# Performance work log

Measured on AMD Instinct MI355X. Metric: run time of the kernel, lower is better.

The kernel has to match this reference:

```python
import jax, jax.numpy as jnp
import numpy as np

ND, NS = 50000, 30000
FD = FS = 256
H = 256
E = 1000000
EL = 200000


def _lin_init(key, fan_in, fan_out):
    # torch Linear default: U(-1/sqrt(fan_in), 1/sqrt(fan_in)) for W and b
    kw, kb = jax.random.split(key)
    bound = 1.0 / np.sqrt(fan_in)
    W = jax.random.uniform(kw, (fan_in, fan_out), jnp.float32, -bound, bound)
    b = jax.random.uniform(kb, (fan_out,), jnp.float32, -bound, bound)
    return W, b


def setup_inputs() -> dict:
    key = jax.random.key(0)
    ks = jax.random.split(key, 16)
    x_drug = jax.random.normal(ks[0], (ND, FD), jnp.float32)
    x_disease = jax.random.normal(ks[1], (NS, FS), jnp.float32)
    edge_src = jax.random.randint(ks[2], (E,), 0, ND, jnp.int64)
    edge_dst = jax.random.randint(ks[3], (E,), 0, NS, jnp.int64)
    label_row = jax.random.randint(ks[4], (EL,), 0, ND, jnp.int64)
    label_col = jax.random.randint(ks[5], (EL,), 0, NS, jnp.int64)
    # SAGEConv params per layer per edge type: lin_l (on aggregated src, with bias),
    # lin_r (on dst root, no bias). Edge types: ds = drug->disease, sd = disease->drug (rev).
    Wl1_ds, bl1_ds = _lin_init(ks[6], FD, H)
    Wr1_ds, _ = _lin_init(ks[7], FS, H)
    Wl1_sd, bl1_sd = _lin_init(ks[8], FS, H)
    Wr1_sd, _ = _lin_init(ks[9], FD, H)
    Wl2_ds, bl2_ds = _lin_init(ks[10], H, H)
    Wr2_ds, _ = _lin_init(ks[11], H, H)
    Wl2_sd, bl2_sd = _lin_init(ks[12], H, H)
    Wr2_sd, _ = _lin_init(ks[13], H, H)
    Wdec1, bdec1 = _lin_init(ks[14], 2 * H, H)
    Wdec2, bdec2 = _lin_init(ks[15], H, 1)
    return dict(x_drug=x_drug, x_disease=x_disease,
                edge_src=edge_src, edge_dst=edge_dst,
                label_row=label_row, label_col=label_col,
                Wl1_ds=Wl1_ds, bl1_ds=bl1_ds, Wr1_ds=Wr1_ds,
                Wl1_sd=Wl1_sd, bl1_sd=bl1_sd, Wr1_sd=Wr1_sd,
                Wl2_ds=Wl2_ds, bl2_ds=bl2_ds, Wr2_ds=Wr2_ds,
                Wl2_sd=Wl2_sd, bl2_sd=bl2_sd, Wr2_sd=Wr2_sd,
                Wdec1=Wdec1, bdec1=bdec1, Wdec2=Wdec2, bdec2=bdec2)


def _mean_agg(x_src, src, dst, n_dst):
    # gather source features per edge, mean-scatter into destinations
    msg = x_src[src]                                         # [E, F]
    s = jax.ops.segment_sum(msg, dst, num_segments=n_dst)    # [n_dst, F]
    cnt = jax.ops.segment_sum(jnp.ones_like(dst, x_src.dtype), dst, num_segments=n_dst)
    return s / jnp.maximum(cnt, 1.0)[:, None]


def _sage_layer(x_drug, x_dis, src, dst,
                Wl_ds, bl_ds, Wr_ds, Wl_sd, bl_sd, Wr_sd):
    z_dis = _mean_agg(x_drug, src, dst, NS) @ Wl_ds + bl_ds + x_dis @ Wr_ds
    z_drug = _mean_agg(x_dis, dst, src, ND) @ Wl_sd + bl_sd + x_drug @ Wr_sd
    return z_drug, z_dis


def reference(x_drug, x_disease, edge_src, edge_dst, label_row, label_col,
              Wl1_ds, bl1_ds, Wr1_ds, Wl1_sd, bl1_sd, Wr1_sd,
              Wl2_ds, bl2_ds, Wr2_ds, Wl2_sd, bl2_sd, Wr2_sd,
              Wdec1, bdec1, Wdec2, bdec2):
    # layer 1 (relu)
    zd, zs = _sage_layer(x_drug, x_disease, edge_src, edge_dst,
                         Wl1_ds, bl1_ds, Wr1_ds, Wl1_sd, bl1_sd, Wr1_sd)
    zd, zs = jax.nn.relu(zd), jax.nn.relu(zs)
    # layer 2 (no relu, last layer)
    zd, zs = _sage_layer(zd, zs, edge_src, edge_dst,
                         Wl2_ds, bl2_ds, Wr2_ds, Wl2_sd, bl2_sd, Wr2_sd)
    # edge decoder
    z = jnp.concatenate([zd[label_row], zs[label_col]], axis=-1)  # [EL, 2H]
    h = jax.nn.relu(z @ Wdec1 + bdec1)
    out = (h @ Wdec2 + bdec2).reshape(-1)
    return out
```

## Files before the change

### kernel.cpp

```cpp
#include <hip/hip_runtime.h>
#include <hip/hip_bf16.h>

#define ND 50000
#define NS 30000
#define NE 1000000
#define EL 200000
#define NTOT (NS + ND)
#define SCAN_BLK ((NTOT + 1023) / 1024)

typedef short short8 __attribute__((ext_vector_type(8)));
typedef float f32x4 __attribute__((ext_vector_type(4)));

__device__ __forceinline__ float b2f(unsigned short u) {
    union { unsigned int i; float f; } c; c.i = ((unsigned int)u) << 16; return c.f;
}
__device__ __forceinline__ unsigned short f2b(float f) {
    __hip_bfloat16 h = __float2bfloat16(f);
    union { __hip_bfloat16 h; unsigned short u; } c; c.h = h; return c.u;
}

__device__ __forceinline__ void gload_lds16(const unsigned short* g, unsigned short* l) {
    __builtin_amdgcn_global_load_lds(
        (const __attribute__((address_space(1))) unsigned int*)g,
        (__attribute__((address_space(3))) unsigned int*)l, 16, 0, 0);
}


__global__ void zero_kernel(int* a, int n) {
    int i = blockIdx.x * blockDim.x + threadIdx.x;
    if (i < n) a[i] = 0;
}

__global__ void rank_kernel(const int* __restrict__ src, const int* __restrict__ dst,
                            int* cnt_drug, int* cnt_dis,
                            unsigned short* __restrict__ rank_sd,
                            unsigned short* __restrict__ rank_ds, int n) {
    int i = blockIdx.x * blockDim.x + threadIdx.x;
    if (i < n) {
        int s = src[i], d = dst[i];
        rank_ds[i] = (unsigned short)atomicAdd(&cnt_dis[d], 1);
        rank_sd[i] = (unsigned short)atomicAdd(&cnt_drug[s], 1);
    }
}

__global__ __launch_bounds__(256) void scan_part(const int* __restrict__ cnt,
                                                 int* __restrict__ bsum) {
    __shared__ int red[4];
    int t = threadIdx.x, lane = t & 63, wid = t >> 6;
    int base = blockIdx.x * 1024 + t * 4;
    int s = 0;
    if (base < NTOT) {
        int4 c = *reinterpret_cast<const int4*>(cnt + base);
        s = c.x + c.y + c.z + c.w;
    }
#pragma unroll
    for (int off = 32; off; off >>= 1) s += __shfl_down(s, off);
    if (lane == 0) red[wid] = s;
    __syncthreads();
    if (t == 0) bsum[blockIdx.x] = red[0] + red[1] + red[2] + red[3];
}

__global__ void scan_top(int* bsum, int nb) {
    int lane = threadIdx.x;
    int a0 = lane < nb ? bsum[lane] : 0;
    int a1 = (64 + lane) < nb ? bsum[64 + lane] : 0;
    int i0 = a0, i1 = a1;
#pragma unroll
    for (int off = 1; off < 64; off <<= 1) {
        int t0 = __shfl_up(i0, off);
        int t1 = __shfl_up(i1, off);
        if (lane >= off) { i0 += t0; i1 += t1; }
    }
    int tot0 = __shfl(i0, 63);
    if (lane < nb) bsum[lane] = i0 - a0;
    if (64 + lane < nb) bsum[64 + lane] = tot0 + i1 - a1;
}

__global__ __launch_bounds__(256) void scan_emit(const int* __restrict__ cnt,
                                                 const int* __restrict__ boff,
                                                 int* __restrict__ row_dis,
                                                 int* __restrict__ row_drug,
                                                 float* __restrict__ inv_dis,
                                                 float* __restrict__ inv_drug) {
    __shared__ int wsum[4];
    int t = threadIdx.x, lane = t & 63, wid = t >> 6;
    int base = blockIdx.x * 1024 + t * 4;
    int4 c = make_int4(0, 0, 0, 0);
    if (base < NTOT) c = *reinterpret_cast<const int4*>(cnt + base);
    int sl = c.x + c.y + c.z + c.w;
    int sc = sl;
#pragma unroll
    for (int off = 1; off < 64; off <<= 1) {
        int tv = __shfl_up(sc, off);
        if (lane >= off) sc += tv;
    }
    if (lane == 63) wsum[wid] = sc;
    __syncthreads();
    int woff = 0;
    for (int w2 = 0; w2 < wid; ++w2) woff += wsum[w2];
    int run = boff[blockIdx.x] + woff + (sc - sl);
    int cc[4] = { c.x, c.y, c.z, c.w };
    if (base < NTOT) {
#pragma unroll
        for (int k = 0; k < 4; ++k) {
            int i = base + k;
            float iv = 1.0f / (float)(cc[k] > 1 ? cc[k] : 1);
            if (i < NS) { row_dis[i] = run; inv_dis[i] = iv; }
            else        { row_drug[i - NS] = run - NE; inv_drug[i - NS] = iv; }
            run += cc[k];
        }
    }
    if (blockIdx.x == 0 && t == 0) { row_dis[NS] = NE; row_drug[ND] = NE; }
}

__global__ void place_kernel(const int* __restrict__ src, const int* __restrict__ dst,
                             const int* __restrict__ row_drug, const int* __restrict__ row_dis,
                             const unsigned short* __restrict__ rank_sd,
                             const unsigned short* __restrict__ rank_ds,
                             unsigned short* __restrict__ val_sd,
                             unsigned short* __restrict__ val_ds, int n) {
    int i = blockIdx.x * blockDim.x + threadIdx.x;
    if (i < n) {
        int s = src[i], d = dst[i];
        val_ds[row_dis[d] + (int)rank_ds[i]] = (unsigned short)s;
        val_sd[row_drug[s] + (int)rank_sd[i]] = (unsigned short)d;
    }
}


__global__ void convert_x(const float* __restrict__ xd, const float* __restrict__ xs,
                          unsigned short* __restrict__ outd, unsigned short* __restrict__ outs) {
    int i = (blockIdx.x * 256 + threadIdx.x) * 4;
    const int NDE = ND * 256;
    if (i < NDE) {
        float4 v = *reinterpret_cast<const float4*>(xd + i);
        ushort4 o; o.x = f2b(v.x); o.y = f2b(v.y); o.z = f2b(v.z); o.w = f2b(v.w);
        *reinterpret_cast<ushort4*>(outd + i) = o;
    } else {
        int j = i - NDE;
        float4 v = *reinterpret_cast<const float4*>(xs + j);
        ushort4 o; o.x = f2b(v.x); o.y = f2b(v.y); o.z = f2b(v.z); o.w = f2b(v.w);
        *reinterpret_cast<ushort4*>(outs + j) = o;
    }
}

struct W10 { const float* p[10]; };

__global__ void transpose_w(W10 s, unsigned short* __restrict__ dst) {
    int o = blockIdx.x * 256 + threadIdx.x;
    int mat = o >> 16, idx = o & 65535;
    int n = idx >> 8, k = idx & 255;
    dst[o] = f2b(s.p[mat][k * 256 + n]);
}


__global__ __launch_bounds__(256) void agg_bf2(const unsigned short* __restrict__ srcDis,
                                               const unsigned short* __restrict__ srcDrug,
                                               const int* __restrict__ row_dis,
                                               const int* __restrict__ row_drug,
                                               const unsigned short* __restrict__ val_ds,
                                               const unsigned short* __restrict__ val_sd,
                                               const float* __restrict__ inv_dis,
                                               const float* __restrict__ inv_drug,
                                               unsigned short* __restrict__ outDis,
                                               unsigned short* __restrict__ outDrug) {
    int wid = threadIdx.x >> 6, lane = threadIdx.x & 63;
    int node = blockIdx.x * 4 + wid;
    const int half = lane >> 5;
    const int sub = lane & 31;
    const unsigned short* xsrc; const int* row; const unsigned short* vals;
    const float* inv; unsigned short* outp;
    if (node < NS) {
        xsrc = srcDis; row = row_dis; vals = val_ds; inv = inv_dis; outp = outDis;
    } else {
        node -= NS;
        if (node >= ND) return;
        xsrc = srcDrug; row = row_drug; vals = val_sd; inv = inv_drug; outp = outDrug;
    }
    const int beg = row[node], end = row[node + 1];
    const int off = sub * 8;
    float a[8] = {};
    int j = beg;
    for (; j + 8 <= end; j += 8) {
        int r0 = vals[j     + half];
        int r1 = vals[j + 2 + half];
        int r2 = vals[j + 4 + half];
        int r3 = vals[j + 6 + half];
        short8 v0 = *reinterpret_cast<const short8*>(xsrc + r0 * 256 + off);
        short8 v1 = *reinterpret_cast<const short8*>(xsrc + r1 * 256 + off);
        short8 v2 = *reinterpret_cast<const short8*>(xsrc + r2 * 256 + off);
        short8 v3 = *reinterpret_cast<const short8*>(xsrc + r3 * 256 + off);
#pragma unroll
        for (int k = 0; k < 8; ++k)
            a[k] += b2f((unsigned short)v0[k]) + b2f((unsigned short)v1[k])
                  + b2f((unsigned short)v2[k]) + b2f((unsigned short)v3[k]);
    }
    for (; j + 2 <= end; j += 2) {
        int r = vals[j + half];
        short8 v = *reinterpret_cast<const short8*>(xsrc + r * 256 + off);
#pragma unroll
        for (int k = 0; k < 8; ++k) a[k] += b2f((unsigned short)v[k]);
    }
    if (j < end && half == 0) {
        int r = vals[j];
        short8 v = *reinterpret_cast<const short8*>(xsrc + r * 256 + off);
#pragma unroll
        for (int k = 0; k < 8; ++k) a[k] += b2f((unsigned short)v[k]);
    }
#pragma unroll
    for (int k = 0; k < 8; ++k) a[k] += __shfl_xor(a[k], 32);
    if (half == 0) {
        const float iv = inv[node];
        short8 o;
#pragma unroll
        for (int k = 0; k < 8; ++k) o[k] = (short)f2b(a[k] * iv);
        *reinterpret_cast<short8*>(outp + node * 256 + off) = o;
    }
}


struct GemmSeg {
    const unsigned short* A1;
    const unsigned short* A2;
    const unsigned short* B1t;
    const unsigned short* B2t;
    const float* bias;
    unsigned short* C;
    int M; int relu; int nblk; int nsteps;
};

__global__ __launch_bounds__(256) void gemm_lds(GemmSeg sa, GemmSeg sb) {
    __shared__ unsigned short As[128 * 64];
    __shared__ unsigned short Bs[128 * 64];
    GemmSeg s;
    int bx = blockIdx.x;
    if (bx < sa.nblk) s = sa;
    else { s = sb; bx -= sa.nblk; }

    const int t = threadIdx.x;
    const int lane = t & 63, w = t >> 6;
    const int wr = w >> 1, wc = w & 1;
    const int fr = lane & 15, g = lane >> 4;
    const int bm0 = bx * 128;
    const int n0b = (int)blockIdx.y * 128;
    const int M = s.M;
    const int r8 = lane >> 3, slotL = lane & 7;

    f32x4 acc[4][4];
#pragma unroll
    for (int m = 0; m < 4; ++m)
#pragma unroll
        for (int n = 0; n < 4; ++n)
            acc[m][n] = (f32x4){0.f, 0.f, 0.f, 0.f};

    for (int st = 0; st < s.nsteps; ++st) {
        const int k0 = (st & 3) * 64;
        const unsigned short* Ap = (st & 4) ? s.A2 : s.A1;
        const unsigned short* Bp = (st & 4) ? s.B2t : s.B1t;
#pragma unroll
        for (int j = 0; j < 4; ++j) {
            const int is = w * 4 + j;
            const int row = is * 8 + r8;
            const int sl = slotL ^ (row & 7);
            int ra = bm0 + row; if (ra >= M) ra = M - 1;
            gload_lds16(Ap + (size_t)ra * 256 + k0 + sl * 8, &As[is * 512]);
            gload_lds16(Bp + (size_t)(n0b + row) * 256 + k0 + sl * 8, &Bs[is * 512]);
        }
        __syncthreads();
#pragma unroll
        for (int kc = 0; kc < 2; ++kc) {
            const int q = kc * 4 + g;
            short8 a[4], b[4];
#pragma unroll
            for (int n = 0; n < 4; ++n) {
                const int br = wc * 64 + n * 16 + fr;
                b[n] = *reinterpret_cast<const short8*>(&Bs[br * 64 + (q ^ (fr & 7)) * 8]);
            }
#pragma unroll
            for (int m = 0; m < 4; ++m) {
                const int ar = wr * 64 + m * 16 + fr;
                a[m] = *reinterpret_cast<const short8*>(&As[ar * 64 + (q ^ (fr & 7)) * 8]);
            }
#pragma unroll
            for (int m = 0; m < 4; ++m)
#pragma unroll
                for (int n = 0; n < 4; ++n)
                    acc[m][n] = __builtin_amdgcn_mfma_f32_16x16x32_bf16(a[m], b[n], acc[m][n], 0, 0, 0);
        }
        __syncthreads();
    }

#pragma unroll
    for (int n = 0; n < 4; ++n) {
        const int col = n0b + wc * 64 + n * 16 + fr;
        const float bv = s.bias ? s.bias[col] : 0.0f;
#pragma unroll
        for (int m = 0; m < 4; ++m) {
#pragma unroll
            for (int r = 0; r < 4; ++r) {
                int row = bm0 + wr * 64 + m * 16 + g * 4 + r;
                if (row < M) {
                    float v = acc[m][n][r] + bv;
                    if (s.relu) v = fmaxf(v, 0.f);
                    s.C[row * 256 + col] = f2b(v);
                }
            }
        }
    }
}


__global__ __launch_bounds__(256) void dec_edge(const unsigned short* __restrict__ Pd,
                                                const unsigned short* __restrict__ Ps,
                                                const int* __restrict__ lrow,
                                                const int* __restrict__ lcol,
                                                const float* __restrict__ b1,
                                                const float* __restrict__ w2,
                                                const float* __restrict__ b2,
                                                float* __restrict__ outp, int n) {
    int wid = threadIdx.x >> 6, lane = threadIdx.x & 63;
    int e = blockIdx.x * 4 + wid;
    if (e >= n) return;
    int r = lrow[e], c = lcol[e];
    const int off = lane * 4;
    ushort4 pd = *reinterpret_cast<const ushort4*>(Pd + r * 256 + off);
    ushort4 ps = *reinterpret_cast<const ushort4*>(Ps + c * 256 + off);
    float4 bb = *reinterpret_cast<const float4*>(b1 + off);
    float4 ww = *reinterpret_cast<const float4*>(w2 + off);
    float s = 0.f;
    s += fmaxf(b2f(pd.x) + b2f(ps.x) + bb.x, 0.f) * ww.x;
    s += fmaxf(b2f(pd.y) + b2f(ps.y) + bb.y, 0.f) * ww.y;
    s += fmaxf(b2f(pd.z) + b2f(ps.z) + bb.z, 0.f) * ww.z;
    s += fmaxf(b2f(pd.w) + b2f(ps.w) + bb.w, 0.f) * ww.w;
#pragma unroll
    for (int o = 32; o; o >>= 1) s += __shfl_down(s, o);
    if (lane == 0) outp[e] = s + b2[0];
}


extern "C" void kernel_launch(void* const* d_in, const int* in_sizes, int n_in,
                              void* d_out, int out_size, void* d_ws, size_t ws_size,
                              hipStream_t stream) {
    const float* x_drug = (const float*)d_in[0];
    const float* x_dis  = (const float*)d_in[1];
    const int* esrc = (const int*)d_in[2];
    const int* edst = (const int*)d_in[3];
    const int* lrow = (const int*)d_in[4];
    const int* lcol = (const int*)d_in[5];
    const float* Wl1_ds = (const float*)d_in[6];
    const float* bl1_ds = (const float*)d_in[7];
    const float* Wr1_ds = (const float*)d_in[8];
    const float* Wl1_sd = (const float*)d_in[9];
    const float* bl1_sd = (const float*)d_in[10];
    const float* Wr1_sd = (const float*)d_in[11];
    const float* Wl2_ds = (const float*)d_in[12];
    const float* bl2_ds = (const float*)d_in[13];
    const float* Wr2_ds = (const float*)d_in[14];
    const float* Wl2_sd = (const float*)d_in[15];
    const float* bl2_sd = (const float*)d_in[16];
    const float* Wr2_sd = (const float*)d_in[17];
    const float* Wdec1 = (const float*)d_in[18];
    const float* bdec1 = (const float*)d_in[19];
    const float* Wdec2 = (const float*)d_in[20];
    const float* bdec2 = (const float*)d_in[21];
    float* outp = (float*)d_out;

    char* ws = (char*)d_ws;
    size_t off = 0;
    auto alloc = [&](size_t bytes) -> void* {
        void* p = ws + off;
        off = (off + bytes + 255) & ~(size_t)255;
        return p;
    };
    int* cnt       = (int*)alloc((size_t)NTOT * 4);
    int* bsum      = (int*)alloc((size_t)SCAN_BLK * 4);
    int* row_dis   = (int*)alloc((size_t)(NS + 1) * 4);
    int* row_drug  = (int*)alloc((size_t)(ND + 1) * 4);
    float* inv_dis = (float*)alloc((size_t)NS * 4);
    float* inv_drug= (float*)alloc((size_t)ND * 4);
    unsigned short* rank_ds = (unsigned short*)alloc((size_t)NE * 2);
    unsigned short* rank_sd = (unsigned short*)alloc((size_t)NE * 2);
    unsigned short* val_ds  = (unsigned short*)alloc((size_t)NE * 2);
    unsigned short* val_sd  = (unsigned short*)alloc((size_t)NE * 2);
    unsigned short* Wt   = (unsigned short*)alloc((size_t)10 * 65536 * 2);
    unsigned short* xd_b = (unsigned short*)alloc((size_t)ND * 256 * 2);
    unsigned short* xs_b = (unsigned short*)alloc((size_t)NS * 256 * 2);
    unsigned short* aggs = (unsigned short*)alloc((size_t)NS * 256 * 2);
    unsigned short* aggd = (unsigned short*)alloc((size_t)ND * 256 * 2);
    unsigned short* zd1  = (unsigned short*)alloc((size_t)ND * 256 * 2);
    unsigned short* zs1  = (unsigned short*)alloc((size_t)NS * 256 * 2);
    unsigned short* zd2  = (unsigned short*)alloc((size_t)ND * 256 * 2);
    unsigned short* zs2  = (unsigned short*)alloc((size_t)NS * 256 * 2);
    unsigned short* Pd   = (unsigned short*)alloc((size_t)ND * 256 * 2);
    unsigned short* Ps   = (unsigned short*)alloc((size_t)NS * 256 * 2);
    int* cnt_dis = cnt;
    int* cnt_drug = cnt + NS;

    convert_x<<<(ND + NS) * 256 / 1024, 256, 0, stream>>>(x_drug, x_dis, xd_b, xs_b);
    W10 wsrc;
    wsrc.p[0] = Wl1_ds; wsrc.p[1] = Wr1_ds; wsrc.p[2] = Wl1_sd; wsrc.p[3] = Wr1_sd;
    wsrc.p[4] = Wl2_ds; wsrc.p[5] = Wr2_ds; wsrc.p[6] = Wl2_sd; wsrc.p[7] = Wr2_sd;
    wsrc.p[8] = Wdec1;
    wsrc.p[9] = Wdec1 + 256 * 256;
    transpose_w<<<2560, 256, 0, stream>>>(wsrc, Wt);
    unsigned short* WT[10];
    for (int i = 0; i < 10; ++i) WT[i] = Wt + (size_t)i * 65536;

    zero_kernel<<<(NTOT + 255) / 256, 256, 0, stream>>>(cnt, NTOT);
    rank_kernel<<<(NE + 255) / 256, 256, 0, stream>>>(esrc, edst, cnt_drug, cnt_dis,
                                                      rank_sd, rank_ds, NE);
    scan_part<<<SCAN_BLK, 256, 0, stream>>>(cnt, bsum);
    scan_top<<<1, 64, 0, stream>>>(bsum, SCAN_BLK);
    scan_emit<<<SCAN_BLK, 256, 0, stream>>>(cnt, bsum, row_dis, row_drug, inv_dis, inv_drug);
    place_kernel<<<(NE + 255) / 256, 256, 0, stream>>>(esrc, edst, row_drug, row_dis,
                                                       rank_sd, rank_ds, val_sd, val_ds, NE);

    const int AGG_GRID = (NTOT + 3) / 4;
    const int NB_NS = (NS + 127) / 128, NB_ND = (ND + 127) / 128;
    dim3 gemm_grid(NB_NS + NB_ND, 2);

    agg_bf2<<<AGG_GRID, 256, 0, stream>>>(xd_b, xs_b, row_dis, row_drug, val_ds, val_sd,
                                          inv_dis, inv_drug, aggs, aggd);
    {
        GemmSeg a = { aggs, xs_b, WT[0], WT[1], bl1_ds, zs1, NS, 1, NB_NS, 8 };
        GemmSeg b = { aggd, xd_b, WT[2], WT[3], bl1_sd, zd1, ND, 1, NB_ND, 8 };
        gemm_lds<<<gemm_grid, 256, 0, stream>>>(a, b);
    }

    agg_bf2<<<AGG_GRID, 256, 0, stream>>>(zd1, zs1, row_dis, row_drug, val_ds, val_sd,
                                          inv_dis, inv_drug, aggs, aggd);
    {
        GemmSeg a = { aggs, zs1, WT[4], WT[5], bl2_ds, zs2, NS, 0, NB_NS, 8 };
        GemmSeg b = { aggd, zd1, WT[6], WT[7], bl2_sd, zd2, ND, 0, NB_ND, 8 };
        gemm_lds<<<gemm_grid, 256, 0, stream>>>(a, b);
    }

    {
        GemmSeg a = { zd2, nullptr, WT[8], nullptr, nullptr, Pd, ND, 0, NB_ND, 4 };
        GemmSeg b = { zs2, nullptr, WT[9], nullptr, nullptr, Ps, NS, 0, NB_NS, 4 };
        gemm_lds<<<gemm_grid, 256, 0, stream>>>(a, b);
    }
    dec_edge<<<(EL + 3) / 4, 256, 0, stream>>>(Pd, Ps, lrow, lcol, bdec1, Wdec2, bdec2, outp, EL);
}
```

Baseline: 575.7 us.

## Split aggregation by feature chunk per XCD with persistent atomic work queues

Replaces the per-node wave aggregation with a persistent kernel that reads the XCC ID and splits the 256-wide feature dimension into eight 32-column chunks. Each chunk is preferentially processed by blocks on one XCD, so that XCD's L2 only has to cache one slice of the source feature table. Blocks pull 32-node groups from per-chunk atomic counters, then move on to other chunks to balance load. The cost is narrower 8-byte gathers, repeated reads of the edge index lists for every chunk, and two __syncthreads plus one atomic per work item.

```diff
diff --git a/kernel.cpp b/kernel.cpp
--- a/kernel.cpp
+++ b/kernel.cpp
@@ -7,6 +7,8 @@
 #define EL 200000
 #define NTOT (NS + ND)
 #define SCAN_BLK ((NTOT + 1023) / 1024)
+#define NCHUNK 8
+#define NGRP (NTOT / 32)
 
 typedef short short8 __attribute__((ext_vector_type(8)));
 typedef float f32x4 __attribute__((ext_vector_type(4)));
@@ -153,8 +155,7 @@
     dst[o] = f2b(s.p[mat][k * 256 + n]);
 }
 
-
-__global__ __launch_bounds__(256) void agg_bf2(const unsigned short* __restrict__ srcDis,
+__global__ __launch_bounds__(256) void agg_xcd(const unsigned short* __restrict__ srcDis,
                                                const unsigned short* __restrict__ srcDrug,
                                                const int* __restrict__ row_dis,
                                                const int* __restrict__ row_drug,
@@ -163,58 +164,57 @@
                                                const float* __restrict__ inv_dis,
                                                const float* __restrict__ inv_drug,
                                                unsigned short* __restrict__ outDis,
-                                               unsigned short* __restrict__ outDrug) {
-    int wid = threadIdx.x >> 6, lane = threadIdx.x & 63;
-    int node = blockIdx.x * 4 + wid;
-    const int half = lane >> 5;
-    const int sub = lane & 31;
-    const unsigned short* xsrc; const int* row; const unsigned short* vals;
-    const float* inv; unsigned short* outp;
-    if (node < NS) {
-        xsrc = srcDis; row = row_dis; vals = val_ds; inv = inv_dis; outp = outDis;
-    } else {
-        node -= NS;
-        if (node >= ND) return;
-        xsrc = srcDrug; row = row_drug; vals = val_sd; inv = inv_drug; outp = outDrug;
-    }
-    const int beg = row[node], end = row[node + 1];
-    const int off = sub * 8;
-    float a[8] = {};
-    int j = beg;
-    for (; j + 8 <= end; j += 8) {
-        int r0 = vals[j     + half];
-        int r1 = vals[j + 2 + half];
-        int r2 = vals[j + 4 + half];
-        int r3 = vals[j + 6 + half];
-        short8 v0 = *reinterpret_cast<const short8*>(xsrc + r0 * 256 + off);
-        short8 v1 = *reinterpret_cast<const short8*>(xsrc + r1 * 256 + off);
-        short8 v2 = *reinterpret_cast<const short8*>(xsrc + r2 * 256 + off);
-        short8 v3 = *reinterpret_cast<const short8*>(xsrc + r3 * 256 + off);
-#pragma unroll
-        for (int k = 0; k < 8; ++k)
-            a[k] += b2f((unsigned short)v0[k]) + b2f((unsigned short)v1[k])
-                  + b2f((unsigned short)v2[k]) + b2f((unsigned short)v3[k]);
-    }
-    for (; j + 2 <= end; j += 2) {
-        int r = vals[j + half];
-        short8 v = *reinterpret_cast<const short8*>(xsrc + r * 256 + off);
-#pragma unroll
-        for (int k = 0; k < 8; ++k) a[k] += b2f((unsigned short)v[k]);
-    }
-    if (j < end && half == 0) {
-        int r = vals[j];
-        short8 v = *reinterpret_cast<const short8*>(xsrc + r * 256 + off);
-#pragma unroll
-        for (int k = 0; k < 8; ++k) a[k] += b2f((unsigned short)v[k]);
-    }
-#pragma unroll
-    for (int k = 0; k < 8; ++k) a[k] += __shfl_xor(a[k], 32);
-    if (half == 0) {
-        const float iv = inv[node];
-        short8 o;
-#pragma unroll
-        for (int k = 0; k < 8; ++k) o[k] = (short)f2b(a[k] * iv);
-        *reinterpret_cast<short8*>(outp + node * 256 + off) = o;
+                                               unsigned short* __restrict__ outDrug,
+                                               int* __restrict__ qcnt) {
+    unsigned xcc;
+    asm volatile("s_getreg_b32 %0, hwreg(HW_REG_XCC_ID)" : "=s"(xcc));
+    xcc &= 7;
+    const int slot = threadIdx.x >> 3;
+    const int sub = threadIdx.x & 7;
+    __shared__ int s_item;
+
+    for (int qi = 0; qi < NCHUNK; ++qi) {
+        const int q = (xcc + qi) & 7;
+        for (;;) {
+            if (threadIdx.x == 0) s_item = atomicAdd(&qcnt[q], 1);
+            __syncthreads();
+            const int g = s_item;
+            __syncthreads();
+            if (g >= NGRP) break;
+            int node = g * 32 + slot;
+            const unsigned short* xsrc; const int* row; const unsigned short* vals;
+            const float* inv; unsigned short* outp;
+            if (node < NS) {
+                xsrc = srcDis; row = row_dis; vals = val_ds; inv = inv_dis; outp = outDis;
+            } else {
+                node -= NS;
+                xsrc = srcDrug; row = row_drug; vals = val_sd; inv = inv_drug; outp = outDrug;
+            }
+            const int beg = row[node], end = row[node + 1];
+            const int off = q * 32 + sub * 4;
+            float a0 = 0.f, a1 = 0.f, a2 = 0.f, a3 = 0.f;
+            int j = beg;
+            for (; j + 4 <= end; j += 4) {
+                int s0 = vals[j], s1 = vals[j + 1], s2 = vals[j + 2], s3 = vals[j + 3];
+                ushort4 v0 = *reinterpret_cast<const ushort4*>(xsrc + s0 * 256 + off);
+                ushort4 v1 = *reinterpret_cast<const ushort4*>(xsrc + s1 * 256 + off);
+                ushort4 v2 = *reinterpret_cast<const ushort4*>(xsrc + s2 * 256 + off);
+                ushort4 v3 = *reinterpret_cast<const ushort4*>(xsrc + s3 * 256 + off);
+                a0 += b2f(v0.x) + b2f(v1.x) + b2f(v2.x) + b2f(v3.x);
+                a1 += b2f(v0.y) + b2f(v1.y) + b2f(v2.y) + b2f(v3.y);
+                a2 += b2f(v0.z) + b2f(v1.z) + b2f(v2.z) + b2f(v3.z);
+                a3 += b2f(v0.w) + b2f(v1.w) + b2f(v2.w) + b2f(v3.w);
+            }
+            for (; j < end; ++j) {
+                int s = vals[j];
+                ushort4 v = *reinterpret_cast<const ushort4*>(xsrc + s * 256 + off);
+                a0 += b2f(v.x); a1 += b2f(v.y); a2 += b2f(v.z); a3 += b2f(v.w);
+            }
+            const float iv = inv[node];
+            ushort4 o;
+            o.x = f2b(a0 * iv); o.y = f2b(a1 * iv); o.z = f2b(a2 * iv); o.w = f2b(a3 * iv);
+            *reinterpret_cast<ushort4*>(outp + node * 256 + off) = o;
+        }
     }
 }
 
@@ -372,7 +372,7 @@
         off = (off + bytes + 255) & ~(size_t)255;
         return p;
     };
-    int* cnt       = (int*)alloc((size_t)NTOT * 4);
+    int* cnt       = (int*)alloc((size_t)(NTOT + 16) * 4);
     int* bsum      = (int*)alloc((size_t)SCAN_BLK * 4);
     int* row_dis   = (int*)alloc((size_t)(NS + 1) * 4);
     int* row_drug  = (int*)alloc((size_t)(ND + 1) * 4);
@@ -395,6 +395,8 @@
     unsigned short* Ps   = (unsigned short*)alloc((size_t)NS * 256 * 2);
     int* cnt_dis = cnt;
     int* cnt_drug = cnt + NS;
+    int* qcnt1 = cnt + NTOT;
+    int* qcnt2 = cnt + NTOT + 8;
 
     convert_x<<<(ND + NS) * 256 / 1024, 256, 0, stream>>>(x_drug, x_dis, xd_b, xs_b);
     W10 wsrc;
@@ -406,7 +408,7 @@
     unsigned short* WT[10];
     for (int i = 0; i < 10; ++i) WT[i] = Wt + (size_t)i * 65536;
 
-    zero_kernel<<<(NTOT + 255) / 256, 256, 0, stream>>>(cnt, NTOT);
+    zero_kernel<<<(NTOT + 16 + 255) / 256, 256, 0, stream>>>(cnt, NTOT + 16);
     rank_kernel<<<(NE + 255) / 256, 256, 0, stream>>>(esrc, edst, cnt_drug, cnt_dis,
                                                       rank_sd, rank_ds, NE);
     scan_part<<<SCAN_BLK, 256, 0, stream>>>(cnt, bsum);
@@ -415,20 +417,20 @@
     place_kernel<<<(NE + 255) / 256, 256, 0, stream>>>(esrc, edst, row_drug, row_dis,
                                                        rank_sd, rank_ds, val_sd, val_ds, NE);
 
-    const int AGG_GRID = (NTOT + 3) / 4;
+    const int AGG_GRID = 2048;
     const int NB_NS = (NS + 127) / 128, NB_ND = (ND + 127) / 128;
     dim3 gemm_grid(NB_NS + NB_ND, 2);
 
-    agg_bf2<<<AGG_GRID, 256, 0, stream>>>(xd_b, xs_b, row_dis, row_drug, val_ds, val_sd,
-                                          inv_dis, inv_drug, aggs, aggd);
+    agg_xcd<<<AGG_GRID, 256, 0, stream>>>(xd_b, xs_b, row_dis, row_drug, val_ds, val_sd,
+                                          inv_dis, inv_drug, aggs, aggd, qcnt1);
     {
         GemmSeg a = { aggs, xs_b, WT[0], WT[1], bl1_ds, zs1, NS, 1, NB_NS, 8 };
         GemmSeg b = { aggd, xd_b, WT[2], WT[3], bl1_sd, zd1, ND, 1, NB_ND, 8 };
         gemm_lds<<<gemm_grid, 256, 0, stream>>>(a, b);
     }
 
-    agg_bf2<<<AGG_GRID, 256, 0, stream>>>(zd1, zs1, row_dis, row_drug, val_ds, val_sd,
-                                          inv_dis, inv_drug, aggs, aggd);
+    agg_xcd<<<AGG_GRID, 256, 0, stream>>>(zd1, zs1, row_dis, row_drug, val_ds, val_sd,
+                                          inv_dis, inv_drug, aggs, aggd, qcnt2);
     {
         GemmSeg a = { aggs, zs1, WT[4], WT[5], bl2_ds, zs2, NS, 0, NB_NS, 8 };
         GemmSeg b = { aggd, zd1, WT[6], WT[7], bl2_sd, zd2, ND, 0, NB_ND, 8 };
```

Result: slower. 1.228 ms (+113.3%).

## Double-buffer LDS tiles in gemm_lds to prefetch next k-step

Applied to the files above, without the earlier changes.

Splits the GEMM's shared-memory A/B tiles into two buffers and issues the global-to-LDS loads for the next k-step before computing on the current one. Row offsets are precomputed once outside the loop. This aims to hide global load latency behind MFMA work, at the cost of doubling LDS usage per block, which may lower occupancy.

```diff
diff --git a/kernel.cpp b/kernel.cpp
--- a/kernel.cpp
+++ b/kernel.cpp
@@ -230,8 +230,8 @@
 };
 
 __global__ __launch_bounds__(256) void gemm_lds(GemmSeg sa, GemmSeg sb) {
-    __shared__ unsigned short As[128 * 64];
-    __shared__ unsigned short Bs[128 * 64];
+    __shared__ unsigned short As[2][128 * 64];
+    __shared__ unsigned short Bs[2][128 * 64];
     GemmSeg s;
     int bx = blockIdx.x;
     if (bx < sa.nblk) s = sa;
@@ -246,6 +246,17 @@
     const int M = s.M;
     const int r8 = lane >> 3, slotL = lane & 7;
 
+    int raOff[4]; int rbOff[4];
+#pragma unroll
+    for (int j = 0; j < 4; ++j) {
+        const int is = w * 4 + j;
+        const int row = is * 8 + r8;
+        const int sl = slotL ^ (row & 7);
+        int ra = bm0 + row; if (ra >= M) ra = M - 1;
+        raOff[j] = ra * 256 + sl * 8;
+        rbOff[j] = (n0b + row) * 256 + sl * 8;
+    }
+
     f32x4 acc[4][4];
 #pragma unroll
     for (int m = 0; m < 4; ++m)
@@ -253,20 +264,32 @@
         for (int n = 0; n < 4; ++n)
             acc[m][n] = (f32x4){0.f, 0.f, 0.f, 0.f};
 
-    for (int st = 0; st < s.nsteps; ++st) {
-        const int k0 = (st & 3) * 64;
-        const unsigned short* Ap = (st & 4) ? s.A2 : s.A1;
-        const unsigned short* Bp = (st & 4) ? s.B2t : s.B1t;
+    const int nsteps = s.nsteps;
+    {
+        const unsigned short* Ap = s.A1;
+        const unsigned short* Bp = s.B1t;
 #pragma unroll
         for (int j = 0; j < 4; ++j) {
             const int is = w * 4 + j;
-            const int row = is * 8 + r8;
-            const int sl = slotL ^ (row & 7);
-            int ra = bm0 + row; if (ra >= M) ra = M - 1;
-            gload_lds16(Ap + (size_t)ra * 256 + k0 + sl * 8, &As[is * 512]);
-            gload_lds16(Bp + (size_t)(n0b + row) * 256 + k0 + sl * 8, &Bs[is * 512]);
+            gload_lds16(Ap + raOff[j], &As[0][is * 512]);
+            gload_lds16(Bp + rbOff[j], &Bs[0][is * 512]);
         }
-        __syncthreads();
+    }
+    __syncthreads();
+
+    for (int st = 0; st < nsteps; ++st) {
+        const int cur = st & 1;
+        if (st + 1 < nsteps) {
+            const int k1 = ((st + 1) & 3) * 64;
+            const unsigned short* Ap = ((st + 1) & 4) ? s.A2 : s.A1;
+            const unsigned short* Bp = ((st + 1) & 4) ? s.B2t : s.B1t;
+#pragma unroll
+            for (int j = 0; j < 4; ++j) {
+                const int is = w * 4 + j;
+                gload_lds16(Ap + raOff[j] + k1, &As[cur ^ 1][is * 512]);
+                gload_lds16(Bp + rbOff[j] + k1, &Bs[cur ^ 1][is * 512]);
+            }
+        }
 #pragma unroll
         for (int kc = 0; kc < 2; ++kc) {
             const int q = kc * 4 + g;
@@ -274,12 +297,12 @@
 #pragma unroll
             for (int n = 0; n < 4; ++n) {
                 const int br = wc * 64 + n * 16 + fr;
-                b[n] = *reinterpret_cast<const short8*>(&Bs[br * 64 + (q ^ (fr & 7)) * 8]);
+                b[n] = *reinterpret_cast<const short8*>(&Bs[cur][br * 64 + (q ^ (fr & 7)) * 8]);
             }
 #pragma unroll
             for (int m = 0; m < 4; ++m) {
                 const int ar = wr * 64 + m * 16 + fr;
-                a[m] = *reinterpret_cast<const short8*>(&As[ar * 64 + (q ^ (fr & 7)) * 8]);
+                a[m] = *reinterpret_cast<const short8*>(&As[cur][ar * 64 + (q ^ (fr & 7)) * 8]);
             }
 #pragma unroll
             for (int m = 0; m < 4; ++m)
```

After: 600.5 us. 4.3% more time.

## Fold decoder first layer into layer-2 weights and merge prep kernels

Applied to the files above, without the earlier changes.

Precomputes the products of the layer-2 SAGE weights with the decoder's first-layer weight halves, plus the layer-2 biases times those halves. Layer 2 can then write the decoder projections Pd/Ps directly, removing the zd2/zs2 intermediates and one full GEMM pass. The rank, bf16 conversion, layer-1 weight transpose and weight-product computations are merged into one multi-role launch to cut launch overhead. The edge decoder now handles two edges per wavefront with 8-wide loads. Precomposing the weights in fp32 and then rounding to bf16 changes the rounding behaviour slightly.

```diff
diff --git a/kernel.cpp b/kernel.cpp
--- a/kernel.cpp
+++ b/kernel.cpp
@@ -8,6 +8,13 @@
 #define NTOT (NS + ND)
 #define SCAN_BLK ((NTOT + 1023) / 1024)
 
+#define RANK_BLKS ((NE + 255) / 256)
+#define CONV_BLKS 20000
+#define TRW4_BLKS 1024
+#define COMP_BLKS 64
+#define BIAS_BLKS 2
+#define MEGA_BLKS (RANK_BLKS + CONV_BLKS + TRW4_BLKS + COMP_BLKS + BIAS_BLKS)
+
 typedef short short8 __attribute__((ext_vector_type(8)));
 typedef float f32x4 __attribute__((ext_vector_type(4)));
 
@@ -25,23 +32,90 @@
         (__attribute__((address_space(3))) unsigned int*)l, 16, 0, 0);
 }
 
+struct WAll {
+    const float* w1[4];
+    const float* w2[4];
+    const float* wdec1;
+    const float* bl2_ds;
+    const float* bl2_sd;
+};
 
 __global__ void zero_kernel(int* a, int n) {
     int i = blockIdx.x * blockDim.x + threadIdx.x;
     if (i < n) a[i] = 0;
 }
 
-__global__ void rank_kernel(const int* __restrict__ src, const int* __restrict__ dst,
-                            int* cnt_drug, int* cnt_dis,
-                            unsigned short* __restrict__ rank_sd,
-                            unsigned short* __restrict__ rank_ds, int n) {
-    int i = blockIdx.x * blockDim.x + threadIdx.x;
-    if (i < n) {
-        int s = src[i], d = dst[i];
-        rank_ds[i] = (unsigned short)atomicAdd(&cnt_dis[d], 1);
-        rank_sd[i] = (unsigned short)atomicAdd(&cnt_drug[s], 1);
-    }
-}
+__global__ __launch_bounds__(256) void mega_prep(const int* __restrict__ esrc,
+                                                 const int* __restrict__ edst,
+                                                 int* cnt_drug, int* cnt_dis,
+                                                 unsigned short* __restrict__ rank_sd,
+                                                 unsigned short* __restrict__ rank_ds,
+                                                 const float* __restrict__ xd,
+                                                 const float* __restrict__ xs,
+                                                 unsigned short* __restrict__ xd_b,
+                                                 unsigned short* __restrict__ xs_b,
+                                                 WAll wa,
+                                                 unsigned short* __restrict__ Wt,
+                                                 float* __restrict__ cbuf) {
+    __shared__ float w2t[16][256];
+    const int b = blockIdx.x, t = threadIdx.x;
+    if (b < RANK_BLKS) {
+        int i = b * 256 + t;
+        if (i < NE) {
+            int s = esrc[i], d = edst[i];
+            rank_ds[i] = (unsigned short)atomicAdd(&cnt_dis[d], 1);
+            rank_sd[i] = (unsigned short)atomicAdd(&cnt_drug[s], 1);
+        }
+    } else if (b < RANK_BLKS + CONV_BLKS) {
+        int i = ((b - RANK_BLKS) * 256 + t) * 4;
+        const int NDE = ND * 256;
+        if (i < NDE) {
+            float4 v = *reinterpret_cast<const float4*>(xd + i);
+            ushort4 o; o.x = f2b(v.x); o.y = f2b(v.y); o.z = f2b(v.z); o.w = f2b(v.w);
+            *reinterpret_cast<ushort4*>(xd_b + i) = o;
+        } else {
+            int j = i - NDE;
+            float4 v = *reinterpret_cast<const float4*>(xs + j);
+            ushort4 o; o.x = f2b(v.x); o.y = f2b(v.y); o.z = f2b(v.z); o.w = f2b(v.w);
+            *reinterpret_cast<ushort4*>(xs_b + j) = o;
+        }
+    } else if (b < RANK_BLKS + CONV_BLKS + TRW4_BLKS) {
+        int o = (b - RANK_BLKS - CONV_BLKS) * 256 + t;
+        int mat = o >> 16, idx = o & 65535;
+        int n = idx >> 8, k = idx & 255;
+        Wt[o] = f2b(wa.w1[mat][k * 256 + n]);
+    } else if (b < RANK_BLKS + CONV_BLKS + TRW4_BLKS + COMP_BLKS) {
+        int cb = b - RANK_BLKS - CONV_BLKS - TRW4_BLKS;
+        int mat = cb >> 4;
+        int k0 = (cb & 15) * 16;
+        const float* W2 = wa.w2[mat];
+        const float* Wd = wa.wdec1 + ((mat < 2) ? 65536 : 0);
+        for (int idx = t; idx < 4096; idx += 256) {
+            int r = idx >> 8, c = idx & 255;
+            w2t[r][c] = W2[(k0 + r) * 256 + c];
+        }
+        __syncthreads();
+        float acc[16] = {};
+        const int n = t;
+        for (int j = 0; j < 256; ++j) {
+            float wd = Wd[j * 256 + n];
+#pragma unroll
+            for (int k = 0; k < 16; ++k) acc[k] += w2t[k][j] * wd;
+        }
+        unsigned short* dst = Wt + (size_t)(4 + mat) * 65536 + n * 256 + k0;
+#pragma unroll
+        for (int k = 0; k < 16; ++k) dst[k] = f2b(acc[k]);
+    } else {
+        int bb = b - RANK_BLKS - CONV_BLKS - TRW4_BLKS - COMP_BLKS;
+        const float* bsrc = bb ? wa.bl2_sd : wa.bl2_ds;
+        const float* Wd = wa.wdec1 + (bb ? 0 : 65536);
+        float acc = 0.f;
+        const int n = t;
+        for (int j = 0; j < 256; ++j) acc += bsrc[j] * Wd[j * 256 + n];
+        cbuf[bb * 256 + n] = acc;
+    }
+}
+
 
 __global__ __launch_bounds__(256) void scan_part(const int* __restrict__ cnt,
                                                  int* __restrict__ bsum) {
@@ -125,32 +199,6 @@
         val_ds[row_dis[d] + (int)rank_ds[i]] = (unsigned short)s;
         val_sd[row_drug[s] + (int)rank_sd[i]] = (unsigned short)d;
     }
-}
-
-
-__global__ void convert_x(const float* __restrict__ xd, const float* __restrict__ xs,
-                          unsigned short* __restrict__ outd, unsigned short* __restrict__ outs) {
-    int i = (blockIdx.x * 256 + threadIdx.x) * 4;
-    const int NDE = ND * 256;
-    if (i < NDE) {
-        float4 v = *reinterpret_cast<const float4*>(xd + i);
-        ushort4 o; o.x = f2b(v.x); o.y = f2b(v.y); o.z = f2b(v.z); o.w = f2b(v.w);
-        *reinterpret_cast<ushort4*>(outd + i) = o;
-    } else {
-        int j = i - NDE;
-        float4 v = *reinterpret_cast<const float4*>(xs + j);
-        ushort4 o; o.x = f2b(v.x); o.y = f2b(v.y); o.z = f2b(v.z); o.w = f2b(v.w);
-        *reinterpret_cast<ushort4*>(outs + j) = o;
-    }
-}
-
-struct W10 { const float* p[10]; };
-
-__global__ void transpose_w(W10 s, unsigned short* __restrict__ dst) {
-    int o = blockIdx.x * 256 + threadIdx.x;
-    int mat = o >> 16, idx = o & 65535;
-    int n = idx >> 8, k = idx & 255;
-    dst[o] = f2b(s.p[mat][k * 256 + n]);
 }
 
 
@@ -319,22 +367,22 @@
                                                 const float* __restrict__ b2,
                                                 float* __restrict__ outp, int n) {
     int wid = threadIdx.x >> 6, lane = threadIdx.x & 63;
-    int e = blockIdx.x * 4 + wid;
+    int half = lane >> 5, sl = lane & 31;
+    int e = blockIdx.x * 8 + wid * 2 + half;
     if (e >= n) return;
     int r = lrow[e], c = lcol[e];
-    const int off = lane * 4;
-    ushort4 pd = *reinterpret_cast<const ushort4*>(Pd + r * 256 + off);
-    ushort4 ps = *reinterpret_cast<const ushort4*>(Ps + c * 256 + off);
-    float4 bb = *reinterpret_cast<const float4*>(b1 + off);
-    float4 ww = *reinterpret_cast<const float4*>(w2 + off);
+    const int off = sl * 8;
+    short8 pd = *reinterpret_cast<const short8*>(Pd + r * 256 + off);
+    short8 ps = *reinterpret_cast<const short8*>(Ps + c * 256 + off);
     float s = 0.f;
-    s += fmaxf(b2f(pd.x) + b2f(ps.x) + bb.x, 0.f) * ww.x;
-    s += fmaxf(b2f(pd.y) + b2f(ps.y) + bb.y, 0.f) * ww.y;
-    s += fmaxf(b2f(pd.z) + b2f(ps.z) + bb.z, 0.f) * ww.z;
-    s += fmaxf(b2f(pd.w) + b2f(ps.w) + bb.w, 0.f) * ww.w;
-#pragma unroll
-    for (int o = 32; o; o >>= 1) s += __shfl_down(s, o);
-    if (lane == 0) outp[e] = s + b2[0];
+#pragma unroll
+    for (int k = 0; k < 8; ++k) {
+        float h = b2f((unsigned short)pd[k]) + b2f((unsigned short)ps[k]) + b1[off + k];
+        s += fmaxf(h, 0.f) * w2[off + k];
+    }
+#pragma unroll
+    for (int o = 16; o; o >>= 1) s += __shfl_down(s, o, 32);
+    if (sl == 0) outp[e] = s + b2[0];
 }
 
 
@@ -378,37 +426,36 @@
     int* row_drug  = (int*)alloc((size_t)(ND + 1) * 4);
     float* inv_dis = (float*)alloc((size_t)NS * 4);
     float* inv_drug= (float*)alloc((size_t)ND * 4);
+    float* cbuf    = (float*)alloc((size_t)512 * 4);
     unsigned short* rank_ds = (unsigned short*)alloc((size_t)NE * 2);
     unsigned short* rank_sd = (unsigned short*)alloc((size_t)NE * 2);
     unsigned short* val_ds  = (unsigned short*)alloc((size_t)NE * 2);
     unsigned short* val_sd  = (unsigned short*)alloc((size_t)NE * 2);
-    unsigned short* Wt   = (unsigned short*)alloc((size_t)10 * 65536 * 2);
+    unsigned short* Wt   = (unsigned short*)alloc((size_t)8 * 65536 * 2);
     unsigned short* xd_b = (unsigned short*)alloc((size_t)ND * 256 * 2);
     unsigned short* xs_b = (unsigned short*)alloc((size_t)NS * 256 * 2);
     unsigned short* aggs = (unsigned short*)alloc((size_t)NS * 256 * 2);
     unsigned short* aggd = (unsigned short*)alloc((size_t)ND * 256 * 2);
     unsigned short* zd1  = (unsigned short*)alloc((size_t)ND * 256 * 2);
     unsigned short* zs1  = (unsigned short*)alloc((size_t)NS * 256 * 2);
-    unsigned short* zd2  = (unsigned short*)alloc((size_t)ND * 256 * 2);
-    unsigned short* zs2  = (unsigned short*)alloc((size_t)NS * 256 * 2);
     unsigned short* Pd   = (unsigned short*)alloc((size_t)ND * 256 * 2);
     unsigned short* Ps   = (unsigned short*)alloc((size_t)NS * 256 * 2);
     int* cnt_dis = cnt;
     int* cnt_drug = cnt + NS;
 
-    convert_x<<<(ND + NS) * 256 / 1024, 256, 0, stream>>>(x_drug, x_dis, xd_b, xs_b);
-    W10 wsrc;
-    wsrc.p[0] = Wl1_ds; wsrc.p[1] = Wr1_ds; wsrc.p[2] = Wl1_sd; wsrc.p[3] = Wr1_sd;
-    wsrc.p[4] = Wl2_ds; wsrc.p[5] = Wr2_ds; wsrc.p[6] = Wl2_sd; wsrc.p[7] = Wr2_sd;
-    wsrc.p[8] = Wdec1;
-    wsrc.p[9] = Wdec1 + 256 * 256;
-    transpose_w<<<2560, 256, 0, stream>>>(wsrc, Wt);
-    unsigned short* WT[10];
-    for (int i = 0; i < 10; ++i) WT[i] = Wt + (size_t)i * 65536;
-
     zero_kernel<<<(NTOT + 255) / 256, 256, 0, stream>>>(cnt, NTOT);
-    rank_kernel<<<(NE + 255) / 256, 256, 0, stream>>>(esrc, edst, cnt_drug, cnt_dis,
-                                                      rank_sd, rank_ds, NE);
+
+    WAll wa;
+    wa.w1[0] = Wl1_ds; wa.w1[1] = Wr1_ds; wa.w1[2] = Wl1_sd; wa.w1[3] = Wr1_sd;
+    wa.w2[0] = Wl2_ds; wa.w2[1] = Wr2_ds; wa.w2[2] = Wl2_sd; wa.w2[3] = Wr2_sd;
+    wa.wdec1 = Wdec1; wa.bl2_ds = bl2_ds; wa.bl2_sd = bl2_sd;
+    mega_prep<<<MEGA_BLKS, 256, 0, stream>>>(esrc, edst, cnt_drug, cnt_dis,
+                                             rank_sd, rank_ds,
+                                             x_drug, x_dis, xd_b, xs_b,
+                                             wa, Wt, cbuf);
+    unsigned short* WT[8];
+    for (int i = 0; i < 8; ++i) WT[i] = Wt + (size_t)i * 65536;
+
     scan_part<<<SCAN_BLK, 256, 0, stream>>>(cnt, bsum);
     scan_top<<<1, 64, 0, stream>>>(bsum, SCAN_BLK);
     scan_emit<<<SCAN_BLK, 256, 0, stream>>>(cnt, bsum, row_dis, row_drug, inv_dis, inv_drug);
@@ -430,15 +477,10 @@
     agg_bf2<<<AGG_GRID, 256, 0, stream>>>(zd1, zs1, row_dis, row_drug, val_ds, val_sd,
                                           inv_dis, inv_drug, aggs, aggd);
     {
-        GemmSeg a = { aggs, zs1, WT[4], WT[5], bl2_ds, zs2, NS, 0, NB_NS, 8 };
-        GemmSeg b = { aggd, zd1, WT[6], WT[7], bl2_sd, zd2, ND, 0, NB_ND, 8 };
+        GemmSeg a = { aggs, zs1, WT[4], WT[5], cbuf,       Ps, NS, 0, NB_NS, 8 };
+        GemmSeg b = { aggd, zd1, WT[6], WT[7], cbuf + 256, Pd, ND, 0, NB_ND, 8 };
         gemm_lds<<<gemm_grid, 256, 0, stream>>>(a, b);
     }
 
-    {
-        GemmSeg a = { zd2, nullptr, WT[8], nullptr, nullptr, Pd, ND, 0, NB_ND, 4 };
-        GemmSeg b = { zs2, nullptr, WT[9], nullptr, nullptr, Ps, NS, 0, NB_NS, 4 };
-        gemm_lds<<<gemm_grid, 256, 0, stream>>>(a, b);
-    }
-    dec_edge<<<(EL + 3) / 4, 256, 0, stream>>>(Pd, Ps, lrow, lcol, bdec1, Wdec2, bdec2, outp, EL);
-}
+    dec_edge<<<(EL + 7) / 8, 256, 0, stream>>>(Pd, Ps, lrow, lcol, bdec1, Wdec2, bdec2, outp, EL);
+}
```

Result: faster. 532.4 us (-7.5%).
